# Performance work log

Hardware: AMD Instinct MI355X
Metric: run time of the kernel (lower is better)

The kernel has to match this reference:

```python
import jax, jax.numpy as jnp
import numpy as np

B, T, I, H, L = 64, 512, 256, 512, 2


def setup_inputs() -> dict:
    key = jax.random.key(0)
    ks = jax.random.split(key, 9)
    std = 1.0 / np.sqrt(H)  # matches reset_parameters uniform(-std, std)
    u = lambda k, shape: jax.random.uniform(k, shape, jnp.float32, -std, std)
    return {
        "x": jax.random.normal(ks[0], (B, T, I), jnp.float32),
        "w_xh0": u(ks[1], (4 * H, I)),  "b_xh0": u(ks[2], (4 * H,)),
        "w_hh0": u(ks[3], (4 * H, H)), "b_hh0": u(ks[4], (4 * H,)),
        "w_xh1": u(ks[5], (4 * H, H)), "b_xh1": u(ks[6], (4 * H,)),
        "w_hh1": u(ks[7], (4 * H, H)), "b_hh1": u(ks[8], (4 * H,)),
    }


def _cell(x, h, c, Wx, bx, Wh, bh):
    # gates = xh(x) + hh(h); chunk order: input, forget, cell, output
    gates = x @ Wx.T + bx + h @ Wh.T + bh
    i, f, g, o = jnp.split(gates, 4, axis=1)
    cy = c * jax.nn.sigmoid(f) + jax.nn.sigmoid(i) * jnp.tanh(g)
    hy = jax.nn.sigmoid(o) * jnp.tanh(cy)
    return hy, cy


def reference(x, w_xh0, b_xh0, w_hh0, b_hh0, w_xh1, b_xh1, w_hh1, b_hh1):
    Bx, Tx, _ = x.shape
    Hx = w_hh0.shape[1]
    params = [(w_xh0, b_xh0, w_hh0, b_hh0), (w_xh1, b_xh1, w_hh1, b_hh1)]
    h0 = jnp.zeros((len(params), Bx, Hx), x.dtype)
    c0 = jnp.zeros((len(params), Bx, Hx), x.dtype)

    def step(carry, xt):
        h, c = carry
        inp = xt
        hs, cs = [], []
        for l, (Wx, bx, Wh, bh) in enumerate(params):
            hy, cy = _cell(inp, h[l], c[l], Wx, bx, Wh, bh)
            hs.append(hy)
            cs.append(cy)
            inp = hy  # dropout p=0.0 -> identity
        return (jnp.stack(hs), jnp.stack(cs)), inp

    (hT, cT), outs = jax.lax.scan(step, (h0, c0), jnp.swapaxes(x, 0, 1))
    return jnp.swapaxes(outs, 0, 1), (hT, cT)
```

## Files before the change

### kernel.cpp

```cpp
#include <hip/hip_runtime.h>
#include <stdint.h>

#define Bn 64
#define Tn 512
#define In 256
#define Hn 512
#define NBLK 64
#define OUT_HT 16777216
#define OUT_CT 16842752
#define LDS_BYTES 131072
#define SLOT_ELEMS (Bn * Hn)
#define DONE_WORDS (2 * 4 * Tn * 32)
#define DONE_BYTES (DONE_WORDS * 4)
#define NSLOT_CAN (Tn + 1)
#define MAX_RETRY (1 << 20)


typedef __attribute__((ext_vector_type(8))) short bf16x8;
typedef __attribute__((ext_vector_type(4))) float f32x4;
typedef unsigned long long u64;

__device__ __forceinline__ unsigned short f2bf(float f) {
    unsigned u = __float_as_uint(f);
    return (unsigned short)((u + 0x7fffu + ((u >> 16) & 1u)) >> 16);
}
__device__ __forceinline__ float sigm(float v) { return 1.0f / (1.0f + __expf(-v)); }
__device__ __forceinline__ float tanhv(float v) { float e = __expf(2.0f * v); return 1.0f - 2.0f / (e + 1.0f); }

__device__ __forceinline__ void stg_coh(unsigned short* p, unsigned short v) {
    __hip_atomic_store(p, v, __ATOMIC_RELAXED, __HIP_MEMORY_SCOPE_AGENT);
}
__device__ __forceinline__ int ld_cnt(const int* p) {
    return __hip_atomic_load(p, __ATOMIC_RELAXED, __HIP_MEMORY_SCOPE_AGENT);
}
__device__ __forceinline__ void st_flag(int* p, int v) {
    __hip_atomic_store(p, v, __ATOMIC_RELAXED, __HIP_MEMORY_SCOPE_AGENT);
}
__device__ __forceinline__ bf16x8 asbf(f32x4 v) {
    union { f32x4 f; bf16x8 h; } u; u.f = v; return u.h;
}
__device__ __forceinline__ unsigned pkminu16(unsigned a, unsigned b) {
    unsigned d;
    asm("v_pk_min_u16 %0, %1, %2" : "=v"(d) : "v"(a), "v"(b));
    return d;
}

#define GLD16_ISSUE(A, VA)                                             \
  asm volatile(                                                        \
    "global_load_dwordx4 %0,  %16, off offset:0 sc0 sc1\n\t"          \
    "global_load_dwordx4 %1,  %16, off offset:64 sc0 sc1\n\t"         \
    "global_load_dwordx4 %2,  %16, off offset:128 sc0 sc1\n\t"        \
    "global_load_dwordx4 %3,  %16, off offset:192 sc0 sc1\n\t"        \
    "global_load_dwordx4 %4,  %16, off offset:256 sc0 sc1\n\t"        \
    "global_load_dwordx4 %5,  %16, off offset:320 sc0 sc1\n\t"        \
    "global_load_dwordx4 %6,  %16, off offset:384 sc0 sc1\n\t"        \
    "global_load_dwordx4 %7,  %16, off offset:448 sc0 sc1\n\t"        \
    "global_load_dwordx4 %8,  %16, off offset:512 sc0 sc1\n\t"        \
    "global_load_dwordx4 %9,  %16, off offset:576 sc0 sc1\n\t"        \
    "global_load_dwordx4 %10, %16, off offset:640 sc0 sc1\n\t"        \
    "global_load_dwordx4 %11, %16, off offset:704 sc0 sc1\n\t"        \
    "global_load_dwordx4 %12, %16, off offset:768 sc0 sc1\n\t"        \
    "global_load_dwordx4 %13, %16, off offset:832 sc0 sc1\n\t"        \
    "global_load_dwordx4 %14, %16, off offset:896 sc0 sc1\n\t"        \
    "global_load_dwordx4 %15, %16, off offset:960 sc0 sc1"             \
    : "=&v"(A[0]), "=&v"(A[1]), "=&v"(A[2]), "=&v"(A[3]),              \
      "=&v"(A[4]), "=&v"(A[5]), "=&v"(A[6]), "=&v"(A[7]),              \
      "=&v"(A[8]), "=&v"(A[9]), "=&v"(A[10]), "=&v"(A[11]),            \
      "=&v"(A[12]), "=&v"(A[13]), "=&v"(A[14]), "=&v"(A[15])           \
    : "v"(VA) : "memory")

#define GLD16X(A, VA)                                                  \
  asm volatile(                                                        \
    "global_load_dwordx4 %0,  %16, off offset:0\n\t"                   \
    "global_load_dwordx4 %1,  %16, off offset:16\n\t"                  \
    "global_load_dwordx4 %2,  %16, off offset:128\n\t"                 \
    "global_load_dwordx4 %3,  %16, off offset:144\n\t"                 \
    "global_load_dwordx4 %4,  %16, off offset:256\n\t"                 \
    "global_load_dwordx4 %5,  %16, off offset:272\n\t"                 \
    "global_load_dwordx4 %6,  %16, off offset:384\n\t"                 \
    "global_load_dwordx4 %7,  %16, off offset:400\n\t"                 \
    "global_load_dwordx4 %8,  %16, off offset:512\n\t"                 \
    "global_load_dwordx4 %9,  %16, off offset:528\n\t"                 \
    "global_load_dwordx4 %10, %16, off offset:640\n\t"                 \
    "global_load_dwordx4 %11, %16, off offset:656\n\t"                 \
    "global_load_dwordx4 %12, %16, off offset:768\n\t"                 \
    "global_load_dwordx4 %13, %16, off offset:784\n\t"                 \
    "global_load_dwordx4 %14, %16, off offset:896\n\t"                 \
    "global_load_dwordx4 %15, %16, off offset:912"                     \
    : "=&v"(A[0]), "=&v"(A[1]), "=&v"(A[2]), "=&v"(A[3]),              \
      "=&v"(A[4]), "=&v"(A[5]), "=&v"(A[6]), "=&v"(A[7]),              \
      "=&v"(A[8]), "=&v"(A[9]), "=&v"(A[10]), "=&v"(A[11]),            \
      "=&v"(A[12]), "=&v"(A[13]), "=&v"(A[14]), "=&v"(A[15])           \
    : "v"(VA) : "memory")

#define VMW(n) do {                                                    \
    asm volatile("s_waitcnt vmcnt(" #n ")" ::: "memory");              \
    __builtin_amdgcn_sched_barrier(0);                                 \
  } while (0)

#define CANCHK(A, OK) do {                                             \
    unsigned m0_ = 0xFFFFFFFFu, m1_ = 0xFFFFFFFFu,                     \
             m2_ = 0xFFFFFFFFu, m3_ = 0xFFFFFFFFu;                     \
    _Pragma("unroll")                                                  \
    for (int i_ = 0; i_ < 16; ++i_) {                                  \
      m0_ = pkminu16(m0_, __float_as_uint(A[i_][0]) ^ 0x7FC17FC1u);    \
      m1_ = pkminu16(m1_, __float_as_uint(A[i_][1]) ^ 0x7FC17FC1u);    \
      m2_ = pkminu16(m2_, __float_as_uint(A[i_][2]) ^ 0x7FC17FC1u);    \
      m3_ = pkminu16(m3_, __float_as_uint(A[i_][3]) ^ 0x7FC17FC1u);    \
    }                                                                  \
    unsigned mt_ = pkminu16(pkminu16(m0_, m1_), pkminu16(m2_, m3_));   \
    OK = __all(((mt_ & 0xFFFFu) != 0u) && ((mt_ >> 16) != 0u));        \
  } while (0)

__global__ void lstm_prep(u64* __restrict__ z0, u64* __restrict__ z1,
                          int* __restrict__ dn, int mode) {
    long tid = (long)blockIdx.x * blockDim.x + threadIdx.x;
    long stride = (long)gridDim.x * blockDim.x;
    if (mode == 0) {
        for (long i = tid; i < DONE_WORDS; i += stride) st_flag(dn + i, 0);
        for (long i = tid; i < SLOT_ELEMS / 4; i += stride) {
            __hip_atomic_store(z0 + i, (u64)0, __ATOMIC_RELAXED, __HIP_MEMORY_SCOPE_AGENT);
            __hip_atomic_store(z1 + i, (u64)0, __ATOMIC_RELAXED, __HIP_MEMORY_SCOPE_AGENT);
        }
    } else {
        const u64 CAN = 0x7FC17FC17FC17FC1ull;
        const long N = (long)NSLOT_CAN * (SLOT_ELEMS / 4);
        for (long i = tid; i < N; i += stride) {
            u64 v = (i < SLOT_ELEMS / 4) ? 0ull : CAN;
            __hip_atomic_store(z0 + i, v, __ATOMIC_RELAXED, __HIP_MEMORY_SCOPE_AGENT);
            __hip_atomic_store(z1 + i, v, __ATOMIC_RELAXED, __HIP_MEMORY_SCOPE_AGENT);
        }
    }
}

#define STAGE_WEIGHTS()                                                      \
    const int I0 = (layer == 0) ? 8 : 16;                                    \
    const int K0 = (layer == 0) ? In : Hn;                                   \
    const float* Wxs = (layer == 0) ? wxh0 : wxh1;                           \
    const float* Whs = (layer == 0) ? whh0 : whh1;                           \
    u64* sm64 = (u64*)smem;                                                  \
    const int tot0 = I0 * 4 * 64;                                            \
    for (int c = threadIdx.x; c < tot0; c += 256) {                          \
        int lc = c & 63, qg = (c >> 6) & 3, ii = c >> 8;                     \
        const float* src = Wxs + (size_t)(qg * Hn + (cb << 4) + (lc & 15)) * K0 \
                               + ii * 32 + (lc >> 4) * 8;                    \
        f32x4 s0 = *(const f32x4*)src;                                       \
        f32x4 s1 = *(const f32x4*)(src + 4);                                 \
        u64 lo = (u64)f2bf(s0[0]) | ((u64)f2bf(s0[1]) << 16) |               \
                 ((u64)f2bf(s0[2]) << 32) | ((u64)f2bf(s0[3]) << 48);        \
        u64 hi = (u64)f2bf(s1[0]) | ((u64)f2bf(s1[1]) << 16) |               \
                 ((u64)f2bf(s1[2]) << 32) | ((u64)f2bf(s1[3]) << 48);        \
        sm64[c * 2] = lo; sm64[c * 2 + 1] = hi;                              \
    }                                                                        \
    const int hbase = tot0;                                                  \
    for (int c = threadIdx.x; c < 16 * 4 * 64; c += 256) {                   \
        int lc = c & 63, qg = (c >> 6) & 3, ii = c >> 8;                     \
        const float* src = Whs + (size_t)(qg * Hn + (cb << 4) + (lc & 15)) * Hn \
                               + ii * 32 + (lc >> 4) * 8;                    \
        f32x4 s0 = *(const f32x4*)src;                                       \
        f32x4 s1 = *(const f32x4*)(src + 4);                                 \
        u64 lo = (u64)f2bf(s0[0]) | ((u64)f2bf(s0[1]) << 16) |               \
                 ((u64)f2bf(s0[2]) << 32) | ((u64)f2bf(s0[3]) << 48);        \
        u64 hi = (u64)f2bf(s1[0]) | ((u64)f2bf(s1[1]) << 16) |               \
                 ((u64)f2bf(s1[2]) << 32) | ((u64)f2bf(s1[3]) << 48);        \
        sm64[(hbase + c) * 2] = lo; sm64[(hbase + c) * 2 + 1] = hi;          \
    }                                                                        \
    __syncthreads();                                                         \
    const bf16x8* bfr = (const bf16x8*)smem;

__launch_bounds__(256, 1)
__global__ void lstm_canary(const float* __restrict__ x,
                            const float* __restrict__ wxh0, const float* __restrict__ whh0,
                            const float* __restrict__ wxh1, const float* __restrict__ whh1,
                            const float* __restrict__ bx0, const float* __restrict__ bh0,
                            const float* __restrict__ bx1, const float* __restrict__ bh1,
                            float* __restrict__ out,
                            unsigned short* __restrict__ h0b,
                            unsigned short* __restrict__ h1b) {
    extern __shared__ char smem[];
    const int layer = blockIdx.x >> 5;
    const int cb    = blockIdx.x & 31;
    const int wv    = threadIdx.x >> 6;
    const int lane  = threadIdx.x & 63;
    const int quad  = lane >> 4;
    const int ln    = lane & 15;
    const int row0  = wv << 4;
    const int colh  = (cb << 4) + ln;

    STAGE_WEIGHTS();

    float bias[4];
#pragma unroll
    for (int q = 0; q < 4; ++q) {
        int gc = q * Hn + colh;
        bias[q] = (layer == 0) ? (bx0[gc] + bh0[gc]) : (bx1[gc] + bh1[gc]);
    }

    const float* xrow0 = x + (size_t)(row0 + ln) * Tn * In + quad * 8;
    const int hoff = (row0 + ln) * Hn + quad * 8;

    float c[4] = {0.f, 0.f, 0.f, 0.f};

    for (int t = 0; t < Tn; ++t) {
        f32x4 acc[4];
#pragma unroll
        for (int q = 0; q < 4; ++q) acc[q] = (f32x4){bias[q], bias[q], bias[q], bias[q]};

        if (layer == 0) {
            const unsigned short* hp = h0b + (size_t)t * SLOT_ELEMS + hoff;
            uint64_t va = (uint64_t)hp;
            f32x4 A[16], xr[16];
            uint64_t vax = (uint64_t)(xrow0 + (size_t)t * In);
            GLD16_ISSUE(A, va);
            GLD16X(xr, vax);
            VMW(16);
            int ok; CANCHK(A, ok);
            int tries = 0;
            while (!ok && ++tries < MAX_RETRY) {
                GLD16_ISSUE(A, va); VMW(0); CANCHK(A, ok);
            }
#pragma unroll
            for (int i = 0; i < 16; ++i)
#pragma unroll
                for (int q = 0; q < 4; ++q)
                    acc[q] = __builtin_amdgcn_mfma_f32_16x16x32_bf16(
                        asbf(A[i]), bfr[hbase + (i * 4 + q) * 64 + lane], acc[q], 0, 0, 0);
            VMW(0);
            bf16x8 axc[8];
#pragma unroll
            for (int i = 0; i < 8; ++i) {
                f32x4 xa = xr[2 * i], xc = xr[2 * i + 1];
                axc[i][0] = (short)f2bf(xa[0]); axc[i][1] = (short)f2bf(xa[1]);
                axc[i][2] = (short)f2bf(xa[2]); axc[i][3] = (short)f2bf(xa[3]);
                axc[i][4] = (short)f2bf(xc[0]); axc[i][5] = (short)f2bf(xc[1]);
                axc[i][6] = (short)f2bf(xc[2]); axc[i][7] = (short)f2bf(xc[3]);
            }
#pragma unroll
            for (int i = 0; i < 8; ++i)
#pragma unroll
                for (int q = 0; q < 4; ++q)
                    acc[q] = __builtin_amdgcn_mfma_f32_16x16x32_bf16(
                        axc[i], bfr[(i * 4 + q) * 64 + lane], acc[q], 0, 0, 0);
        } else {
            const unsigned short* p0 = h0b + (size_t)(t + 1) * SLOT_ELEMS + hoff;
            const unsigned short* p1 = h1b + (size_t)t * SLOT_ELEMS + hoff;
            uint64_t va = (uint64_t)p0, vb = (uint64_t)p1;
            f32x4 A[16], Bv[16];
            GLD16_ISSUE(A, va);
            GLD16_ISSUE(Bv, vb);
            VMW(16);
            int ok; CANCHK(A, ok);
            int tries = 0;
            while (!ok && ++tries < MAX_RETRY) {
                GLD16_ISSUE(A, va); VMW(0); CANCHK(A, ok);
            }
#pragma unroll
            for (int i = 0; i < 16; ++i)
#pragma unroll
                for (int q = 0; q < 4; ++q)
                    acc[q] = __builtin_amdgcn_mfma_f32_16x16x32_bf16(
                        asbf(A[i]), bfr[(i * 4 + q) * 64 + lane], acc[q], 0, 0, 0);
            VMW(0);
            CANCHK(Bv, ok);
            tries = 0;
            while (!ok && ++tries < MAX_RETRY) {
                GLD16_ISSUE(Bv, vb); VMW(0); CANCHK(Bv, ok);
            }
#pragma unroll
            for (int i = 0; i < 16; ++i)
#pragma unroll
                for (int q = 0; q < 4; ++q)
                    acc[q] = __builtin_amdgcn_mfma_f32_16x16x32_bf16(
                        asbf(Bv[i]), bfr[hbase + (i * 4 + q) * 64 + lane], acc[q], 0, 0, 0);
        }

        unsigned short* hw = ((layer == 0) ? h0b : h1b) + (size_t)(t + 1) * SLOT_ELEMS;
        float hv[4];
#pragma unroll
        for (int r = 0; r < 4; ++r) {
            int row = row0 + quad * 4 + r;
            float ig = sigm(acc[0][r]);
            float fg = sigm(acc[1][r]);
            float gg = tanhv(acc[2][r]);
            float og = sigm(acc[3][r]);
            float cy = c[r] * fg + ig * gg;
            float hy = og * tanhv(cy);
            c[r] = cy;
            hv[r] = hy;
            stg_coh(hw + row * Hn + colh, f2bf(hy));
        }
        if (layer == 1) {
#pragma unroll
            for (int r = 0; r < 4; ++r) {
                int row = row0 + quad * 4 + r;
                out[(size_t)row * (Tn * Hn) + (size_t)t * Hn + colh] = hv[r];
            }
        }
        if (t == Tn - 1) {
#pragma unroll
            for (int r = 0; r < 4; ++r) {
                int row = row0 + quad * 4 + r;
                out[OUT_HT + layer * (Bn * Hn) + row * Hn + colh] = hv[r];
                out[OUT_CT + layer * (Bn * Hn) + row * Hn + colh] = c[r];
            }
        }
    }
}

__launch_bounds__(256, 1)
__global__ void lstm_flags(const float* __restrict__ x,
                           const float* __restrict__ wxh0, const float* __restrict__ whh0,
                           const float* __restrict__ wxh1, const float* __restrict__ whh1,
                           const float* __restrict__ bx0, const float* __restrict__ bh0,
                           const float* __restrict__ bx1, const float* __restrict__ bh1,
                           float* __restrict__ out,
                           unsigned short* __restrict__ h0b,
                           unsigned short* __restrict__ h1b,
                           int* __restrict__ done, int nslot) {
    extern __shared__ char smem[];
    const int layer = blockIdx.x >> 5;
    const int cb    = blockIdx.x & 31;
    const int wv    = threadIdx.x >> 6;
    const int lane  = threadIdx.x & 63;
    const int quad  = lane >> 4;
    const int ln    = lane & 15;
    const int row0  = wv << 4;
    const int colh  = (cb << 4) + ln;

    STAGE_WEIGHTS();

    float bias[4];
#pragma unroll
    for (int q = 0; q < 4; ++q) {
        int gc = q * Hn + colh;
        bias[q] = (layer == 0) ? (bx0[gc] + bh0[gc]) : (bx1[gc] + bh1[gc]);
    }

    const float* xrow0 = x + (size_t)(row0 + ln) * Tn * In + quad * 8;
    const int hoff = (row0 + ln) * Hn + quad * 8;

    const int lm = lane & 31;
    const int* d0 = done + ((0 * 4 + wv) * Tn) * 32 + lm;
    const int* d1 = done + ((1 * 4 + wv) * Tn) * 32 + lm;
    int* pub = done + ((layer * 4 + wv) * Tn) * 32 + cb;

    float c[4] = {0.f, 0.f, 0.f, 0.f};
    int rs = 0, wsl = 1;
    int gdone = -1;

    for (int t = 0; t < Tn; ++t) {
        f32x4 acc[4];
#pragma unroll
        for (int q = 0; q < 4; ++q) acc[q] = (f32x4){bias[q], bias[q], bias[q], bias[q]};

        if (layer == 0) {
            const float* xp = xrow0 + (size_t)t * In;
            f32x4 xr[16];
#pragma unroll
            for (int i = 0; i < 8; ++i) {
                xr[2 * i]     = *(const f32x4*)(xp + i * 32);
                xr[2 * i + 1] = *(const f32x4*)(xp + i * 32 + 4);
            }
            bf16x8 axc[8];
#pragma unroll
            for (int i = 0; i < 8; ++i) {
                f32x4 xa = xr[2 * i], xc = xr[2 * i + 1];
                axc[i][0] = (short)f2bf(xa[0]); axc[i][1] = (short)f2bf(xa[1]);
                axc[i][2] = (short)f2bf(xa[2]); axc[i][3] = (short)f2bf(xa[3]);
                axc[i][4] = (short)f2bf(xc[0]); axc[i][5] = (short)f2bf(xc[1]);
                axc[i][6] = (short)f2bf(xc[2]); axc[i][7] = (short)f2bf(xc[3]);
            }
#pragma unroll
            for (int i = 0; i < 8; ++i)
#pragma unroll
                for (int q = 0; q < 4; ++q)
                    acc[q] = __builtin_amdgcn_mfma_f32_16x16x32_bf16(
                        axc[i], bfr[(i * 4 + q) * 64 + lane], acc[q], 0, 0, 0);

            {
                int g = t + 1 - nslot;
                if (g >= 0 && g > gdone) {
                    int probe = g + 32; if (probe > Tn - 1) probe = Tn - 1;
                    if (__all(ld_cnt(d1 + probe * 32) > 0)) gdone = probe;
                    else {
                        const int* gp = d1 + g * 32;
                        while (!__all(ld_cnt(gp) > 0)) __builtin_amdgcn_s_sleep(4);
                        gdone = g;
                    }
                }
            }
            if (t > 0) {
                const int* p = d0 + (t - 1) * 32;
                while (!__all(ld_cnt(p) > 0)) { }
            }
            asm volatile("" ::: "memory");

            const unsigned short* hp = h0b + (size_t)rs * SLOT_ELEMS + hoff;
            f32x4 A[16];
            uint64_t va = (uint64_t)hp;
            GLD16_ISSUE(A, va);
            VMW(12);
#pragma unroll
            for (int i = 0; i < 4; ++i)
#pragma unroll
                for (int q = 0; q < 4; ++q)
                    acc[q] = __builtin_amdgcn_mfma_f32_16x16x32_bf16(
                        asbf(A[i]), bfr[hbase + (i * 4 + q) * 64 + lane], acc[q], 0, 0, 0);
            VMW(8);
#pragma unroll
            for (int i = 4; i < 8; ++i)
#pragma unroll
                for (int q = 0; q < 4; ++q)
                    acc[q] = __builtin_amdgcn_mfma_f32_16x16x32_bf16(
                        asbf(A[i]), bfr[hbase + (i * 4 + q) * 64 + lane], acc[q], 0, 0, 0);
            VMW(4);
#pragma unroll
            for (int i = 8; i < 12; ++i)
#pragma unroll
                for (int q = 0; q < 4; ++q)
                    acc[q] = __builtin_amdgcn_mfma_f32_16x16x32_bf16(
                        asbf(A[i]), bfr[hbase + (i * 4 + q) * 64 + lane], acc[q], 0, 0, 0);
            VMW(0);
#pragma unroll
            for (int i = 12; i < 16; ++i)
#pragma unroll
                for (int q = 0; q < 4; ++q)
                    acc[q] = __builtin_amdgcn_mfma_f32_16x16x32_bf16(
                        asbf(A[i]), bfr[hbase + (i * 4 + q) * 64 + lane], acc[q], 0, 0, 0);
        } else {
            {
                const int* p = d0 + t * 32;
                while (!__all(ld_cnt(p) > 0)) { }
            }
            asm volatile("" ::: "memory");
            const unsigned short* p0 = h0b + (size_t)wsl * SLOT_ELEMS + hoff;
            f32x4 A[16], Bv[16];
            uint64_t va = (uint64_t)p0;
            GLD16_ISSUE(A, va);
            if (t > 0) {
                const int* p = d1 + (t - 1) * 32;
                while (!__all(ld_cnt(p) > 0)) { }
            }
            asm volatile("" ::: "memory");
            const unsigned short* p1 = h1b + (size_t)rs * SLOT_ELEMS + hoff;
            uint64_t vb = (uint64_t)p1;
            GLD16_ISSUE(Bv, vb);
            VMW(28);
#pragma unroll
            for (int i = 0; i < 4; ++i)
#pragma unroll
                for (int q = 0; q < 4; ++q)
                    acc[q] = __builtin_amdgcn_mfma_f32_16x16x32_bf16(
                        asbf(A[i]), bfr[(i * 4 + q) * 64 + lane], acc[q], 0, 0, 0);
            VMW(24);
#pragma unroll
            for (int i = 4; i < 8; ++i)
#pragma unroll
                for (int q = 0; q < 4; ++q)
                    acc[q] = __builtin_amdgcn_mfma_f32_16x16x32_bf16(
                        asbf(A[i]), bfr[(i * 4 + q) * 64 + lane], acc[q], 0, 0, 0);
            VMW(20);
#pragma unroll
            for (int i = 8; i < 12; ++i)
#pragma unroll
                for (int q = 0; q < 4; ++q)
                    acc[q] = __builtin_amdgcn_mfma_f32_16x16x32_bf16(
                        asbf(A[i]), bfr[(i * 4 + q) * 64 + lane], acc[q], 0, 0, 0);
            VMW(16);
#pragma unroll
            for (int i = 12; i < 16; ++i)
#pragma unroll
                for (int q = 0; q < 4; ++q)
                    acc[q] = __builtin_amdgcn_mfma_f32_16x16x32_bf16(
                        asbf(A[i]), bfr[(i * 4 + q) * 64 + lane], acc[q], 0, 0, 0);
            VMW(12);
#pragma unroll
            for (int i = 0; i < 4; ++i)
#pragma unroll
                for (int q = 0; q < 4; ++q)
                    acc[q] = __builtin_amdgcn_mfma_f32_16x16x32_bf16(
                        asbf(Bv[i]), bfr[hbase + (i * 4 + q) * 64 + lane], acc[q], 0, 0, 0);
            VMW(8);
#pragma unroll
            for (int i = 4; i < 8; ++i)
#pragma unroll
                for (int q = 0; q < 4; ++q)
                    acc[q] = __builtin_amdgcn_mfma_f32_16x16x32_bf16(
                        asbf(Bv[i]), bfr[hbase + (i * 4 + q) * 64 + lane], acc[q], 0, 0, 0);
            VMW(4);
#pragma unroll
            for (int i = 8; i < 12; ++i)
#pragma unroll
                for (int q = 0; q < 4; ++q)
                    acc[q] = __builtin_amdgcn_mfma_f32_16x16x32_bf16(
                        asbf(Bv[i]), bfr[hbase + (i * 4 + q) * 64 + lane], acc[q], 0, 0, 0);
            VMW(0);
#pragma unroll
            for (int i = 12; i < 16; ++i)
#pragma unroll
                for (int q = 0; q < 4; ++q)
                    acc[q] = __builtin_amdgcn_mfma_f32_16x16x32_bf16(
                        asbf(Bv[i]), bfr[hbase + (i * 4 + q) * 64 + lane], acc[q], 0, 0, 0);
        }

        unsigned short* hw = ((layer == 0) ? h0b : h1b) + (size_t)wsl * SLOT_ELEMS;
        float hv[4];
#pragma unroll
        for (int r = 0; r < 4; ++r) {
            int row = row0 + quad * 4 + r;
            float ig = sigm(acc[0][r]);
            float fg = sigm(acc[1][r]);
            float gg = tanhv(acc[2][r]);
            float og = sigm(acc[3][r]);
            float cy = c[r] * fg + ig * gg;
            float hy = og * tanhv(cy);
            c[r] = cy;
            hv[r] = hy;
            stg_coh(hw + row * Hn + colh, f2bf(hy));
        }
        asm volatile("s_waitcnt vmcnt(0)" ::: "memory");
        if (lane == 0) st_flag(pub + t * 32, t + 1);

        if (layer == 1) {
#pragma unroll
            for (int r = 0; r < 4; ++r) {
                int row = row0 + quad * 4 + r;
                out[(size_t)row * (Tn * Hn) + (size_t)t * Hn + colh] = hv[r];
            }
        }
        if (t == Tn - 1) {
#pragma unroll
            for (int r = 0; r < 4; ++r) {
                int row = row0 + quad * 4 + r;
                out[OUT_HT + layer * (Bn * Hn) + row * Hn + colh] = hv[r];
                out[OUT_CT + layer * (Bn * Hn) + row * Hn + colh] = c[r];
            }
        }

        rs = wsl;
        wsl = (wsl + 1 == nslot) ? 0 : wsl + 1;
    }
}

extern "C" void kernel_launch(void* const* d_in, const int* in_sizes, int n_in,
                              void* d_out, int out_size, void* d_ws, size_t ws_size,
                              hipStream_t stream) {
    const float* x    = (const float*)d_in[0];
    const float* wxh0 = (const float*)d_in[1];
    const float* bxh0 = (const float*)d_in[2];
    const float* whh0 = (const float*)d_in[3];
    const float* bhh0 = (const float*)d_in[4];
    const float* wxh1 = (const float*)d_in[5];
    const float* bxh1 = (const float*)d_in[6];
    const float* whh1 = (const float*)d_in[7];
    const float* bhh1 = (const float*)d_in[8];
    float* out = (float*)d_out;

    char* ws = (char*)d_ws;
    int* done = (int*)ws;
    unsigned short* h0b = (unsigned short*)(ws + DONE_BYTES);

    static int lds_attr_set = 0;
    if (!lds_attr_set) {
        hipFuncSetAttribute((const void*)lstm_canary,
                            hipFuncAttributeMaxDynamicSharedMemorySize, LDS_BYTES);
        hipFuncSetAttribute((const void*)lstm_flags,
                            hipFuncAttributeMaxDynamicSharedMemorySize, LDS_BYTES);
        lds_attr_set = 1;
    }

    const size_t need_can = (size_t)DONE_BYTES
                          + 2ull * NSLOT_CAN * SLOT_ELEMS * 2 + 64;
    if (ws_size >= need_can) {
        unsigned short* h1b = h0b + (size_t)NSLOT_CAN * SLOT_ELEMS;
        lstm_prep<<<dim3(1024), dim3(256), 0, stream>>>(
            (u64*)h0b, (u64*)h1b, done, 1);
        lstm_canary<<<dim3(NBLK), dim3(256), LDS_BYTES, stream>>>(
            x, wxh0, whh0, wxh1, whh1, bxh0, bhh0, bxh1, bhh1, out, h0b, h1b);
    } else {
        long nslot_l = (long)((ws_size - DONE_BYTES) / (2 * (size_t)SLOT_ELEMS * 2));
        int nslot = (int)(nslot_l < 3 ? 3 : (nslot_l > Tn + 1 ? Tn + 1 : nslot_l));
        unsigned short* h1b = h0b + (size_t)nslot * SLOT_ELEMS;
        lstm_prep<<<dim3(256), dim3(256), 0, stream>>>(
            (u64*)h0b, (u64*)h1b, done, 0);
        lstm_flags<<<dim3(NBLK), dim3(256), LDS_BYTES, stream>>>(
            x, wxh0, whh0, wxh1, whh1, bxh0, bhh0, bxh1, bhh1,
            out, h0b, h1b, done, nslot);
    }
}
```

Baseline: 3.562 ms.

## Consume hidden-state chunks incrementally and reload only unready chunks

Replaces the all-or-nothing readiness check on the recurrent h slices with a per-chunk check. Each chunk is fed into MFMA as soon as it no longer holds the canary pattern, and only the missing chunks are reloaded. Layer 0 now does the x-projection MFMAs first, which gives the h data more time to arrive. Layer 1 waits on both loads before consuming. The aim is to cut polling latency and redundant reloads in the cross-block wavefront sync, at the cost of more branchy control flow and register pressure, and it risks serializing MFMAs behind per-chunk wave-wide votes.

```diff
diff --git a/kernel.cpp b/kernel.cpp
--- a/kernel.cpp
+++ b/kernel.cpp
@@ -14,6 +14,7 @@
 #define DONE_BYTES (DONE_WORDS * 4)
 #define NSLOT_CAN (Tn + 1)
 #define MAX_RETRY (1 << 20)
+#define CANC 0x7FC17FC1u
 
 
 typedef __attribute__((ext_vector_type(8))) short bf16x8;
@@ -98,18 +99,51 @@
     __builtin_amdgcn_sched_barrier(0);                                 \
   } while (0)
 
-#define CANCHK(A, OK) do {                                             \
-    unsigned m0_ = 0xFFFFFFFFu, m1_ = 0xFFFFFFFFu,                     \
-             m2_ = 0xFFFFFFFFu, m3_ = 0xFFFFFFFFu;                     \
-    _Pragma("unroll")                                                  \
-    for (int i_ = 0; i_ < 16; ++i_) {                                  \
-      m0_ = pkminu16(m0_, __float_as_uint(A[i_][0]) ^ 0x7FC17FC1u);    \
-      m1_ = pkminu16(m1_, __float_as_uint(A[i_][1]) ^ 0x7FC17FC1u);    \
-      m2_ = pkminu16(m2_, __float_as_uint(A[i_][2]) ^ 0x7FC17FC1u);    \
-      m3_ = pkminu16(m3_, __float_as_uint(A[i_][3]) ^ 0x7FC17FC1u);    \
+#define CHK1(A, idx, OKI) do {                                         \
+    unsigned c0_ = __float_as_uint(A[idx][0]) ^ CANC;                  \
+    unsigned c1_ = __float_as_uint(A[idx][1]) ^ CANC;                  \
+    unsigned c2_ = __float_as_uint(A[idx][2]) ^ CANC;                  \
+    unsigned c3_ = __float_as_uint(A[idx][3]) ^ CANC;                  \
+    unsigned mm_ = pkminu16(pkminu16(c0_, c1_), pkminu16(c2_, c3_));   \
+    OKI = __all(((mm_ & 0xFFFFu) != 0u) && ((mm_ >> 16) != 0u));       \
+  } while (0)
+
+#define RF1(A, VA, idx, off)                                           \
+    if (miss_ & (1u << idx)) {                                         \
+      asm volatile("global_load_dwordx4 %0, %1, off offset:" #off      \
+                   " sc0 sc1" : "=&v"(A[idx]) : "v"(VA) : "memory");   \
+    }
+#define RELOAD_MISS(A, VA)                                             \
+    RF1(A, VA, 0, 0)    RF1(A, VA, 1, 64)   RF1(A, VA, 2, 128)         \
+    RF1(A, VA, 3, 192)  RF1(A, VA, 4, 256)  RF1(A, VA, 5, 320)         \
+    RF1(A, VA, 6, 384)  RF1(A, VA, 7, 448)  RF1(A, VA, 8, 512)         \
+    RF1(A, VA, 9, 576)  RF1(A, VA, 10, 640) RF1(A, VA, 11, 704)        \
+    RF1(A, VA, 12, 768) RF1(A, VA, 13, 832) RF1(A, VA, 14, 896)        \
+    RF1(A, VA, 15, 960)
+
+#define CONSUME_INC(A, VA, WB0) do {                                   \
+    unsigned miss_ = 0xFFFFu;                                          \
+    int tries_ = 0;                                                    \
+    for (;;) {                                                         \
+      _Pragma("unroll")                                                \
+      for (int i_ = 0; i_ < 16; ++i_) {                                \
+        if (miss_ & (1u << i_)) {                                      \
+          int oki_;                                                    \
+          CHK1(A, i_, oki_);                                           \
+          if (oki_) {                                                  \
+            _Pragma("unroll")                                          \
+            for (int q_ = 0; q_ < 4; ++q_)                             \
+              acc[q_] = __builtin_amdgcn_mfma_f32_16x16x32_bf16(       \
+                  asbf(A[i_]), bfr[(WB0) + (i_ * 4 + q_) * 64 + lane], \
+                  acc[q_], 0, 0, 0);                                   \
+            miss_ &= ~(1u << i_);                                      \
+          }                                                            \
+        }                                                              \
+      }                                                                \
+      if (!miss_ || ++tries_ >= MAX_RETRY) break;                      \
+      RELOAD_MISS(A, VA);                                              \
+      VMW(0);                                                          \
     }                                                                  \
-    unsigned mt_ = pkminu16(pkminu16(m0_, m1_), pkminu16(m2_, m3_));   \
-    OK = __all(((mt_ & 0xFFFFu) != 0u) && ((mt_ >> 16) != 0u));        \
   } while (0)
 
 __global__ void lstm_prep(u64* __restrict__ z0, u64* __restrict__ z1,
@@ -213,18 +247,6 @@
             uint64_t vax = (uint64_t)(xrow0 + (size_t)t * In);
             GLD16_ISSUE(A, va);
             GLD16X(xr, vax);
-            VMW(16);
-            int ok; CANCHK(A, ok);
-            int tries = 0;
-            while (!ok && ++tries < MAX_RETRY) {
-                GLD16_ISSUE(A, va); VMW(0); CANCHK(A, ok);
-            }
-#pragma unroll
-            for (int i = 0; i < 16; ++i)
-#pragma unroll
-                for (int q = 0; q < 4; ++q)
-                    acc[q] = __builtin_amdgcn_mfma_f32_16x16x32_bf16(
-                        asbf(A[i]), bfr[hbase + (i * 4 + q) * 64 + lane], acc[q], 0, 0, 0);
             VMW(0);
             bf16x8 axc[8];
 #pragma unroll
@@ -241,37 +263,17 @@
                 for (int q = 0; q < 4; ++q)
                     acc[q] = __builtin_amdgcn_mfma_f32_16x16x32_bf16(
                         axc[i], bfr[(i * 4 + q) * 64 + lane], acc[q], 0, 0, 0);
+            CONSUME_INC(A, va, hbase);
         } else {
             const unsigned short* p0 = h0b + (size_t)(t + 1) * SLOT_ELEMS + hoff;
             const unsigned short* p1 = h1b + (size_t)t * SLOT_ELEMS + hoff;
             uint64_t va = (uint64_t)p0, vb = (uint64_t)p1;
             f32x4 A[16], Bv[16];
+            GLD16_ISSUE(Bv, vb);
             GLD16_ISSUE(A, va);
-            GLD16_ISSUE(Bv, vb);
-            VMW(16);
-            int ok; CANCHK(A, ok);
-            int tries = 0;
-            while (!ok && ++tries < MAX_RETRY) {
-                GLD16_ISSUE(A, va); VMW(0); CANCHK(A, ok);
-            }
-#pragma unroll
-            for (int i = 0; i < 16; ++i)
-#pragma unroll
-                for (int q = 0; q < 4; ++q)
-                    acc[q] = __builtin_amdgcn_mfma_f32_16x16x32_bf16(
-                        asbf(A[i]), bfr[(i * 4 + q) * 64 + lane], acc[q], 0, 0, 0);
             VMW(0);
-            CANCHK(Bv, ok);
-            tries = 0;
-            while (!ok && ++tries < MAX_RETRY) {
-                GLD16_ISSUE(Bv, vb); VMW(0); CANCHK(Bv, ok);
-            }
-#pragma unroll
-            for (int i = 0; i < 16; ++i)
-#pragma unroll
-                for (int q = 0; q < 4; ++q)
-                    acc[q] = __builtin_amdgcn_mfma_f32_16x16x32_bf16(
-                        asbf(Bv[i]), bfr[hbase + (i * 4 + q) * 64 + lane], acc[q], 0, 0, 0);
+            CONSUME_INC(A, va, 0);
+            CONSUME_INC(Bv, vb, hbase);
         }
 
         unsigned short* hw = ((layer == 0) ? h0b : h1b) + (size_t)(t + 1) * SLOT_ELEMS;
```

New measurement: 4.967 ms. +39.4%, slower.
